# Optimization experiments

Hardware: AMD Instinct MI355X
Metric: run time of the kernel (lower is better)

## Reference

```python
import jax, jax.numpy as jnp
import numpy as np

N = 100000
E = 3200000
IN_DIM = 128
HID = 64
BN_EPS = 1e-5


def _gcn_conv(x, W, b, src, dst, dinv):
    h = x @ W                                      # [N, out]
    coeff = (dinv[src] * dinv[dst])[:, None]       # [E, 1]
    msg = h[src] * coeff                           # gather over edges
    agg = jax.ops.segment_sum(msg, dst, num_segments=N)
    agg = agg + h * (dinv * dinv)[:, None]         # self-loop term
    return agg + b


def setup_inputs() -> dict:
    key = jax.random.key(0)
    ks = jax.random.split(key, 12)
    x = jax.random.normal(ks[0], (N, IN_DIM), dtype=jnp.float32)
    edge_index = jax.random.randint(ks[1], (2, E), 0, N, dtype=jnp.int64)
    s1 = 1.0 / np.sqrt(IN_DIM)
    s2 = 1.0 / np.sqrt(HID)
    W1 = jax.random.uniform(ks[2], (IN_DIM, HID), jnp.float32, -s1, s1)
    b1 = jnp.zeros((HID,), jnp.float32)
    W2 = jax.random.uniform(ks[3], (HID, HID), jnp.float32, -s2, s2)
    b2 = jnp.zeros((HID,), jnp.float32)
    W3 = jax.random.uniform(ks[4], (HID, 1), jnp.float32, -s2, s2)
    b3 = jnp.zeros((1,), jnp.float32)
    g1 = jnp.ones((HID,), jnp.float32)
    beta1 = jnp.zeros((HID,), jnp.float32)
    m1 = 0.1 * jax.random.normal(ks[5], (HID,), jnp.float32)
    v1 = jax.random.uniform(ks[6], (HID,), jnp.float32) + 0.5
    g2 = jnp.ones((HID,), jnp.float32)
    beta2 = jnp.zeros((HID,), jnp.float32)
    m2 = 0.1 * jax.random.normal(ks[7], (HID,), jnp.float32)
    v2 = jax.random.uniform(ks[8], (HID,), jnp.float32) + 0.5
    return {"x": x, "edge_index": edge_index,
            "W1": W1, "b1": b1, "W2": W2, "b2": b2, "W3": W3, "b3": b3,
            "g1": g1, "beta1": beta1, "m1": m1, "v1": v1,
            "g2": g2, "beta2": beta2, "m2": m2, "v2": v2}


def reference(x, edge_index, W1, b1, W2, b2, W3, b3,
              g1, beta1, m1, v1, g2, beta2, m2, v2):
    src, dst = edge_index[0], edge_index[1]
    # degree with self-loops (computed on destination index, PyG convention)
    deg = jax.ops.segment_sum(jnp.ones((E,), jnp.float32), dst, num_segments=N) + 1.0
    dinv = jax.lax.rsqrt(deg)

    def bn(h, g, beta, m, v):
        return (h - m) * jax.lax.rsqrt(v + BN_EPS) * g + beta

    h = _gcn_conv(x, W1, b1, src, dst, dinv)
    h = jax.nn.relu(bn(h, g1, beta1, m1, v1))  # dropout is a no-op in eval
    h = _gcn_conv(h, W2, b2, src, dst, dinv)
    h = jax.nn.relu(bn(h, g2, beta2, m2, v2))
    h = _gcn_conv(h, W3, b3, src, dst, dinv)
    return jax.nn.sigmoid(h)  # [N, 1]
```

## Files before the change

kernel.cpp:

```cpp
#include <hip/hip_runtime.h>
#include <math.h>

#define N_NODES 100000
#define E_EDGES 3200000
#define IN_DIM_ 128
#define HID_ 64
#define BN_EPS_ 1e-5f

#define PB 200
#define CHUNK 16000
#define NBUCK 391

typedef __attribute__((ext_vector_type(8))) short short8;
typedef __attribute__((ext_vector_type(4))) float f32x4;

__device__ inline ushort f2bf(float f) {
    union { float f; unsigned u; } c; c.f = f;
    unsigned r = c.u + 0x7fff + ((c.u >> 16) & 1);
    return (ushort)(r >> 16);
}
__device__ inline float bf_lo(unsigned p) { union { unsigned u; float f; } c; c.u = p << 16; return c.f; }
__device__ inline float bf_hi(unsigned p) { union { unsigned u; float f; } c; c.u = p & 0xffff0000u; return c.f; }

__global__ __launch_bounds__(256) void passA1_hist(const int* __restrict__ ei,
                                                   int* __restrict__ histPB) {
    __shared__ int hist[NBUCK];
    int t = threadIdx.x, b = blockIdx.x;
    for (int k = t; k < NBUCK; k += 256) hist[k] = 0;
    __syncthreads();
    int e0 = b * CHUNK, e1 = e0 + CHUNK;
    for (int e = e0 + t; e < e1; e += 256) {
        int d = ei[E_EDGES + e];
        atomicAdd(&hist[d >> 8], 1);
    }
    __syncthreads();
    for (int k = t; k < NBUCK; k += 256) histPB[k * PB + b] = hist[k];
}

__global__ __launch_bounds__(256) void scan_rows(int* __restrict__ histPB,
                                                 int* __restrict__ bucket_tot) {
    __shared__ int wsum[4];
    int k = blockIdx.x, t = threadIdx.x, lane = t & 63, wv = t >> 6;
    int v = (t < PB) ? histPB[k * PB + t] : 0;
    int s = v;
#pragma unroll
    for (int off = 1; off < 64; off <<= 1) {
        int u = __shfl_up(s, off, 64);
        if (lane >= off) s += u;
    }
    if (lane == 63) wsum[wv] = s;
    __syncthreads();
    int wbase = 0;
    for (int w = 0; w < wv; w++) wbase += wsum[w];
    if (t < PB) histPB[k * PB + t] = wbase + s - v;
    if (t == 255) bucket_tot[k] = wbase + s;
}

__global__ __launch_bounds__(512) void scan_totals(const int* __restrict__ bucket_tot,
                                                   int* __restrict__ bucket_base,
                                                   int* __restrict__ row_ptr) {
    __shared__ int wsum[8];
    int t = threadIdx.x, lane = t & 63, wv = t >> 6;
    int v = (t < NBUCK) ? bucket_tot[t] : 0;
    int s = v;
#pragma unroll
    for (int off = 1; off < 64; off <<= 1) {
        int u = __shfl_up(s, off, 64);
        if (lane >= off) s += u;
    }
    if (lane == 63) wsum[wv] = s;
    __syncthreads();
    int wbase = 0;
    for (int w = 0; w < wv; w++) wbase += wsum[w];
    if (t < NBUCK) bucket_base[t] = wbase + s - v;
    if (t == 0) {
        bucket_base[NBUCK] = E_EDGES;
        row_ptr[N_NODES] = E_EDGES;
    }
}

__global__ __launch_bounds__(256) void passA2_scatter(const int* __restrict__ ei,
                                                      const int* __restrict__ histPB,
                                                      const int* __restrict__ bucket_base,
                                                      int* __restrict__ ebuf) {
    __shared__ int cur[NBUCK];
    int t = threadIdx.x, b = blockIdx.x;
    for (int k = t; k < NBUCK; k += 256) cur[k] = bucket_base[k] + histPB[k * PB + b];
    __syncthreads();
    int e0 = b * CHUNK, e1 = e0 + CHUNK;
    for (int e = e0 + t; e < e1; e += 256) {
        int s = ei[e];
        int d = ei[E_EDGES + e];
        int bk = d >> 8;
        int pos = atomicAdd(&cur[bk], 1);
        ebuf[pos] = s | ((d & 255) << 17);
    }
}

__global__ __launch_bounds__(256) void passB_place(const int* __restrict__ ebuf,
                                                   const int* __restrict__ bucket_base,
                                                   int* __restrict__ row_ptr,
                                                   int* __restrict__ csr_src,
                                                   float* __restrict__ dinv) {
    __shared__ int hist[256];
    __shared__ int wsum[4];
    int b = blockIdx.x, t = threadIdx.x, lane = t & 63, wv = t >> 6;
    int base = bucket_base[b], end = bucket_base[b + 1];
    hist[t] = 0;
    __syncthreads();
    for (int k = base + t; k < end; k += 256)
        atomicAdd(&hist[ebuf[k] >> 17], 1);
    __syncthreads();
    int v = hist[t];
    int s = v;
#pragma unroll
    for (int off = 1; off < 64; off <<= 1) {
        int u = __shfl_up(s, off, 64);
        if (lane >= off) s += u;
    }
    if (lane == 63) wsum[wv] = s;
    __syncthreads();
    int wbase = 0;
    for (int w = 0; w < wv; w++) wbase += wsum[w];
    int excl = wbase + s - v;
    int node = b * 256 + t;
    if (node < N_NODES) {
        row_ptr[node] = base + excl;
        dinv[node] = rsqrtf((float)v + 1.0f);
    }
    __syncthreads();
    hist[t] = excl;
    __syncthreads();
    for (int k = base + t; k < end; k += 256) {
        int pv = ebuf[k];
        int pos = atomicAdd(&hist[pv >> 17], 1);
        csr_src[base + pos] = pv & 0x1FFFF;
    }
}

template<int K, bool BF16IN>
__global__ __launch_bounds__(256) void gemm_bf16(const void* __restrict__ Xv,
                                                 const float* __restrict__ W,
                                                 const float* __restrict__ dinv,
                                                 ushort* __restrict__ hs) {
    constexpr int KP = K + 8;
    __shared__ ushort A_lds[64][KP];
    __shared__ ushort Wt_lds[64][KP];
    int t = threadIdx.x;
    long row0 = (long)blockIdx.x * 64;

    for (int i = t; i < K * 16; i += 256) {
        float4 w4 = ((const float4*)W)[i];
        int k = i >> 4, n = (i & 15) * 4;
        Wt_lds[n + 0][k] = f2bf(w4.x);
        Wt_lds[n + 1][k] = f2bf(w4.y);
        Wt_lds[n + 2][k] = f2bf(w4.z);
        Wt_lds[n + 3][k] = f2bf(w4.w);
    }
    if (BF16IN) {
        constexpr int K2 = K / 2;
        const unsigned* X = (const unsigned*)Xv;
        for (int i = t; i < 64 * K2; i += 256) {
            int r = i / K2, c = i % K2;
            unsigned val = 0;
            long row = row0 + r;
            if (row < N_NODES) val = X[row * K2 + c];
            *(unsigned*)&A_lds[r][c * 2] = val;
        }
    } else {
        constexpr int K4 = K / 4;
        const float* X = (const float*)Xv;
        for (int i = t; i < 64 * K4; i += 256) {
            int r = i / K4, c = i % K4;
            float4 val = make_float4(0.f, 0.f, 0.f, 0.f);
            long row = row0 + r;
            if (row < N_NODES) val = ((const float4*)X)[row * K4 + c];
            int cb = c * 4;
            A_lds[r][cb + 0] = f2bf(val.x);
            A_lds[r][cb + 1] = f2bf(val.y);
            A_lds[r][cb + 2] = f2bf(val.z);
            A_lds[r][cb + 3] = f2bf(val.w);
        }
    }
    __syncthreads();

    int w = t >> 6, l = t & 63;
    int m = l & 15, quad = l >> 4;
    f32x4 acc[4];
#pragma unroll
    for (int c = 0; c < 4; c++) acc[c] = (f32x4){0.f, 0.f, 0.f, 0.f};

#pragma unroll
    for (int ch = 0; ch < K / 32; ch++) {
        short8 a = *(const short8*)&A_lds[16 * w + m][32 * ch + 8 * quad];
#pragma unroll
        for (int c = 0; c < 4; c++) {
            short8 b = *(const short8*)&Wt_lds[16 * c + m][32 * ch + 8 * quad];
            acc[c] = __builtin_amdgcn_mfma_f32_16x16x32_bf16(a, b, acc[c], 0, 0, 0);
        }
    }

#pragma unroll
    for (int r = 0; r < 4; r++) {
        long node = row0 + 16 * w + quad * 4 + r;
        if (node < N_NODES) {
            float dv = dinv[node];
#pragma unroll
            for (int c = 0; c < 4; c++)
                hs[node * 64 + 16 * c + m] = f2bf(acc[c][r] * dv);
        }
    }
}

template<bool LAST>
__global__ __launch_bounds__(256) void gather_feat(const int* __restrict__ row_ptr,
                                                   const int* __restrict__ csr_src,
                                                   const ushort* __restrict__ hs,
                                                   const float* __restrict__ dinv,
                                                   const float* __restrict__ b,
                                                   const float* __restrict__ g,
                                                   const float* __restrict__ beta,
                                                   const float* __restrict__ m,
                                                   const float* __restrict__ v,
                                                   unsigned* __restrict__ y,
                                                   const float* __restrict__ W3,
                                                   float* __restrict__ hs3, int n) {
    int i = (blockIdx.x * 256 + threadIdx.x) >> 6;
    if (i >= n) return;
    int l = threadIdx.x & 63;
    int half = l >> 5, u = l & 31;
    const unsigned* H = (const unsigned*)hs;
    int beg = row_ptr[i], end = row_ptr[i + 1];
    float a0 = 0.f, a1 = 0.f;
    int k = beg + half;
    for (; k + 6 < end; k += 8) {
        int s0 = csr_src[k], s1 = csr_src[k + 2], s2 = csr_src[k + 4], s3 = csr_src[k + 6];
        unsigned p0 = H[s0 * 32 + u], p1 = H[s1 * 32 + u];
        unsigned p2 = H[s2 * 32 + u], p3 = H[s3 * 32 + u];
        a0 += (bf_lo(p0) + bf_lo(p1)) + (bf_lo(p2) + bf_lo(p3));
        a1 += (bf_hi(p0) + bf_hi(p1)) + (bf_hi(p2) + bf_hi(p3));
    }
    for (; k < end; k += 2) {
        unsigned p = H[csr_src[k] * 32 + u];
        a0 += bf_lo(p);
        a1 += bf_hi(p);
    }
    a0 += __shfl_xor(a0, 32, 64);
    a1 += __shfl_xor(a1, 32, 64);
    unsigned ps = H[(long)i * 32 + u];
    a0 += bf_lo(ps);
    a1 += bf_hi(ps);

    float2 bb = ((const float2*)b)[u];
    float2 gg = ((const float2*)g)[u];
    float2 be = ((const float2*)beta)[u];
    float2 mm = ((const float2*)m)[u];
    float2 vv = ((const float2*)v)[u];
    float di = dinv[i];
    float s0 = gg.x * rsqrtf(vv.x + BN_EPS_);
    float s1 = gg.y * rsqrtf(vv.y + BN_EPS_);
    float o0 = fmaxf((di * a0 + bb.x - mm.x) * s0 + be.x, 0.f);
    float o1 = fmaxf((di * a1 + bb.y - mm.y) * s1 + be.y, 0.f);

    if (LAST) {
        float2 w3 = ((const float2*)W3)[u];
        float p = o0 * w3.x + o1 * w3.y;
#pragma unroll
        for (int off = 16; off > 0; off >>= 1)
            p += __shfl_down(p, off, 32);
        if (l == 0) hs3[i] = p * di;
    } else {
        if (half == 0)
            y[(long)i * 32 + u] = (unsigned)f2bf(o0) | ((unsigned)f2bf(o1) << 16);
    }
}

__global__ __launch_bounds__(256) void gather3(const int* __restrict__ row_ptr,
                                               const int* __restrict__ csr_src,
                                               const float* __restrict__ hs3,
                                               const float* __restrict__ dinv,
                                               const float* __restrict__ b3,
                                               float* __restrict__ out, int n) {
    int i = blockIdx.x * 256 + threadIdx.x;
    if (i >= n) return;
    int beg = row_ptr[i], end = row_ptr[i + 1];
    float s0 = hs3[i], s1 = 0.f, s2 = 0.f, s3 = 0.f;
    float s4 = 0.f, s5 = 0.f, s6 = 0.f, s7 = 0.f;
    int k = beg;
    for (; k + 8 <= end; k += 8) {
        s0 += hs3[csr_src[k]];
        s1 += hs3[csr_src[k + 1]];
        s2 += hs3[csr_src[k + 2]];
        s3 += hs3[csr_src[k + 3]];
        s4 += hs3[csr_src[k + 4]];
        s5 += hs3[csr_src[k + 5]];
        s6 += hs3[csr_src[k + 6]];
        s7 += hs3[csr_src[k + 7]];
    }
    for (; k < end; k++) s0 += hs3[csr_src[k]];
    float z = dinv[i] * (((s0 + s1) + (s2 + s3)) + ((s4 + s5) + (s6 + s7))) + b3[0];
    out[i] = 1.f / (1.f + expf(-z));
}

extern "C" void kernel_launch(void* const* d_in, const int* in_sizes, int n_in,
                              void* d_out, int out_size, void* d_ws, size_t ws_size,
                              hipStream_t stream) {
    const int N = N_NODES;
    const int E = E_EDGES;

    const float* x   = (const float*)d_in[0];
    const int*   ei  = (const int*)d_in[1];
    const float* W1  = (const float*)d_in[2];
    const float* b1  = (const float*)d_in[3];
    const float* W2  = (const float*)d_in[4];
    const float* b2  = (const float*)d_in[5];
    const float* W3  = (const float*)d_in[6];
    const float* b3  = (const float*)d_in[7];
    const float* g1  = (const float*)d_in[8];
    const float* bt1 = (const float*)d_in[9];
    const float* m1  = (const float*)d_in[10];
    const float* v1  = (const float*)d_in[11];
    const float* g2  = (const float*)d_in[12];
    const float* bt2 = (const float*)d_in[13];
    const float* m2  = (const float*)d_in[14];
    const float* v2  = (const float*)d_in[15];
    float* out = (float*)d_out;

    int*    wsi         = (int*)d_ws;
    float*  dinv        = (float*)wsi;
    float*  hs3         = (float*)(wsi + (long)N);
    int*    row_ptr     = wsi + 2L * N;
    int*    histPB      = wsi + 3L * N + 16;
    int*    bucket_tot  = histPB + NBUCK * PB;
    int*    bucket_base = bucket_tot + 400;
    int*    csr_src     = bucket_base + 400;
    ushort* hsb         = (ushort*)(csr_src + (long)E);
    unsigned* yb        = (unsigned*)(csr_src + (long)E + 32L * N);
    int*    ebuf        = (int*)hsb;

    passA1_hist<<<PB, 256, 0, stream>>>(ei, histPB);
    scan_rows<<<NBUCK, 256, 0, stream>>>(histPB, bucket_tot);
    scan_totals<<<1, 512, 0, stream>>>(bucket_tot, bucket_base, row_ptr);
    passA2_scatter<<<PB, 256, 0, stream>>>(ei, histPB, bucket_base, ebuf);
    passB_place<<<NBUCK, 256, 0, stream>>>(ebuf, bucket_base, row_ptr, csr_src, dinv);

    gemm_bf16<IN_DIM_, false><<<(N + 63) / 64, 256, 0, stream>>>(x, W1, dinv, hsb);
    gather_feat<false><<<N / 4, 256, 0, stream>>>(row_ptr, csr_src, hsb, dinv,
                                                  b1, g1, bt1, m1, v1, yb, W3, hs3, N);
    gemm_bf16<HID_, true><<<(N + 63) / 64, 256, 0, stream>>>(yb, W2, dinv, hsb);
    gather_feat<true><<<N / 4, 256, 0, stream>>>(row_ptr, csr_src, hsb, dinv,
                                                 b2, g2, bt2, m2, v2, yb, W3, hs3, N);
    gather3<<<(N + 255) / 256, 256, 0, stream>>>(row_ptr, csr_src, hs3, dinv, b3, out, N);
}
```

Before: 435.1 us.

## Sort CSR neighbors by source range and unroll gather loop to 8 loads

The CSR placement pass now sub-buckets each destination node's edges into six source-index ranges, so neighbor lists come out roughly ordered by source node. Gathers across the wave then hit nearby rows of the feature table at about the same time, which should improve L2 locality. The aggregation loop is also unrolled from 4 to 8 outstanding gathers per half-wave to raise memory-level parallelism. Costs are a larger LDS histogram, an integer divide per edge in the placement pass, and more registers in the aggregation kernel.

```diff
diff --git a/kernel.cpp b/kernel.cpp
--- a/kernel.cpp
+++ b/kernel.cpp
@@ -10,6 +10,9 @@
 #define PB 200
 #define CHUNK 16000
 #define NBUCK 391
+
+#define CCH 6
+#define CNODES 16667
 
 typedef __attribute__((ext_vector_type(8))) short short8;
 typedef __attribute__((ext_vector_type(4))) float f32x4;
@@ -102,17 +105,24 @@
                                                    int* __restrict__ row_ptr,
                                                    int* __restrict__ csr_src,
                                                    float* __restrict__ dinv) {
-    __shared__ int hist[256];
+    __shared__ int hist[256 * CCH];
     __shared__ int wsum[4];
     int b = blockIdx.x, t = threadIdx.x, lane = t & 63, wv = t >> 6;
     int base = bucket_base[b], end = bucket_base[b + 1];
-    hist[t] = 0;
-    __syncthreads();
-    for (int k = base + t; k < end; k += 256)
-        atomicAdd(&hist[ebuf[k] >> 17], 1);
-    __syncthreads();
-    int v = hist[t];
-    int s = v;
+    for (int k = t; k < 256 * CCH; k += 256) hist[k] = 0;
+    __syncthreads();
+    for (int k = base + t; k < end; k += 256) {
+        int pv = ebuf[k];
+        int nd = (pv >> 17) & 255;
+        int c = (pv & 0x1FFFF) / CNODES;
+        atomicAdd(&hist[nd * CCH + c], 1);
+    }
+    __syncthreads();
+    int v[CCH];
+    int tot = 0;
+#pragma unroll
+    for (int c = 0; c < CCH; c++) { v[c] = hist[t * CCH + c]; tot += v[c]; }
+    int s = tot;
 #pragma unroll
     for (int off = 1; off < 64; off <<= 1) {
         int u = __shfl_up(s, off, 64);
@@ -122,18 +132,24 @@
     __syncthreads();
     int wbase = 0;
     for (int w = 0; w < wv; w++) wbase += wsum[w];
-    int excl = wbase + s - v;
+    int excl = wbase + s - tot;
     int node = b * 256 + t;
     if (node < N_NODES) {
         row_ptr[node] = base + excl;
-        dinv[node] = rsqrtf((float)v + 1.0f);
-    }
-    __syncthreads();
-    hist[t] = excl;
+        dinv[node] = rsqrtf((float)tot + 1.0f);
+    }
+    int run = excl;
+#pragma unroll
+    for (int c = 0; c < CCH; c++) {
+        hist[t * CCH + c] = run;
+        run += v[c];
+    }
     __syncthreads();
     for (int k = base + t; k < end; k += 256) {
         int pv = ebuf[k];
-        int pos = atomicAdd(&hist[pv >> 17], 1);
+        int nd = (pv >> 17) & 255;
+        int c = (pv & 0x1FFFF) / CNODES;
+        int pos = atomicAdd(&hist[nd * CCH + c], 1);
         csr_src[base + pos] = pv & 0x1FFFF;
     }
 }
@@ -233,12 +249,17 @@
     int beg = row_ptr[i], end = row_ptr[i + 1];
     float a0 = 0.f, a1 = 0.f;
     int k = beg + half;
-    for (; k + 6 < end; k += 8) {
-        int s0 = csr_src[k], s1 = csr_src[k + 2], s2 = csr_src[k + 4], s3 = csr_src[k + 6];
+    for (; k + 14 < end; k += 16) {
+        int s0 = csr_src[k],      s1 = csr_src[k + 2],  s2 = csr_src[k + 4],  s3 = csr_src[k + 6];
+        int s4 = csr_src[k + 8],  s5 = csr_src[k + 10], s6 = csr_src[k + 12], s7 = csr_src[k + 14];
         unsigned p0 = H[s0 * 32 + u], p1 = H[s1 * 32 + u];
         unsigned p2 = H[s2 * 32 + u], p3 = H[s3 * 32 + u];
-        a0 += (bf_lo(p0) + bf_lo(p1)) + (bf_lo(p2) + bf_lo(p3));
-        a1 += (bf_hi(p0) + bf_hi(p1)) + (bf_hi(p2) + bf_hi(p3));
+        unsigned p4 = H[s4 * 32 + u], p5 = H[s5 * 32 + u];
+        unsigned p6 = H[s6 * 32 + u], p7 = H[s7 * 32 + u];
+        a0 += ((bf_lo(p0) + bf_lo(p1)) + (bf_lo(p2) + bf_lo(p3))) +
+              ((bf_lo(p4) + bf_lo(p5)) + (bf_lo(p6) + bf_lo(p7)));
+        a1 += ((bf_hi(p0) + bf_hi(p1)) + (bf_hi(p2) + bf_hi(p3))) +
+              ((bf_hi(p4) + bf_hi(p5)) + (bf_hi(p6) + bf_hi(p7)));
     }
     for (; k < end; k += 2) {
         unsigned p = H[csr_src[k] * 32 + u];
```

Measured after the change: 438.6 us. Within noise of the previous version (+0.8%).

## Gather 16-byte feature slices over 8 edges per wave in GCN aggregation

Applied to the files above, without the earlier changes.

Restructures the per-node gather so each 64-lane wave processes 8 edges at once, with each lane loading a 16-byte uint4 slice (8 bf16 features) rather than 4 bytes. Partial sums are combined across edge slots with xor shuffles, and the bias, batch-norm and output stages are widened to match. The aim is fewer, wider memory requests and more edges in flight per iteration for low-degree nodes. The cost is more registers and a longer shuffle reduction, and lanes sit idle in the tail when a node's degree is not a multiple of 8.

```diff
diff --git a/kernel.cpp b/kernel.cpp
--- a/kernel.cpp
+++ b/kernel.cpp
@@ -228,50 +228,94 @@
     int i = (blockIdx.x * 256 + threadIdx.x) >> 6;
     if (i >= n) return;
     int l = threadIdx.x & 63;
-    int half = l >> 5, u = l & 31;
-    const unsigned* H = (const unsigned*)hs;
+    int es = l >> 3, fg = l & 7;
+    const uint4* H4 = (const uint4*)hs;
+
+    float a0 = 0.f, a1 = 0.f, a2 = 0.f, a3 = 0.f;
+    float a4 = 0.f, a5 = 0.f, a6 = 0.f, a7 = 0.f;
+
+    if (es == 0) {
+        uint4 p = H4[(long)i * 8 + fg];
+        a0 += bf_lo(p.x); a1 += bf_hi(p.x);
+        a2 += bf_lo(p.y); a3 += bf_hi(p.y);
+        a4 += bf_lo(p.z); a5 += bf_hi(p.z);
+        a6 += bf_lo(p.w); a7 += bf_hi(p.w);
+    }
+
     int beg = row_ptr[i], end = row_ptr[i + 1];
-    float a0 = 0.f, a1 = 0.f;
-    int k = beg + half;
-    for (; k + 6 < end; k += 8) {
-        int s0 = csr_src[k], s1 = csr_src[k + 2], s2 = csr_src[k + 4], s3 = csr_src[k + 6];
-        unsigned p0 = H[s0 * 32 + u], p1 = H[s1 * 32 + u];
-        unsigned p2 = H[s2 * 32 + u], p3 = H[s3 * 32 + u];
-        a0 += (bf_lo(p0) + bf_lo(p1)) + (bf_lo(p2) + bf_lo(p3));
-        a1 += (bf_hi(p0) + bf_hi(p1)) + (bf_hi(p2) + bf_hi(p3));
-    }
-    for (; k < end; k += 2) {
-        unsigned p = H[csr_src[k] * 32 + u];
-        a0 += bf_lo(p);
-        a1 += bf_hi(p);
-    }
-    a0 += __shfl_xor(a0, 32, 64);
-    a1 += __shfl_xor(a1, 32, 64);
-    unsigned ps = H[(long)i * 32 + u];
-    a0 += bf_lo(ps);
-    a1 += bf_hi(ps);
-
-    float2 bb = ((const float2*)b)[u];
-    float2 gg = ((const float2*)g)[u];
-    float2 be = ((const float2*)beta)[u];
-    float2 mm = ((const float2*)m)[u];
-    float2 vv = ((const float2*)v)[u];
+    int k = beg;
+    for (; k + 16 <= end; k += 16) {
+        int sA = csr_src[k + es];
+        int sB = csr_src[k + 8 + es];
+        uint4 pA = H4[(long)sA * 8 + fg];
+        uint4 pB = H4[(long)sB * 8 + fg];
+        a0 += bf_lo(pA.x) + bf_lo(pB.x); a1 += bf_hi(pA.x) + bf_hi(pB.x);
+        a2 += bf_lo(pA.y) + bf_lo(pB.y); a3 += bf_hi(pA.y) + bf_hi(pB.y);
+        a4 += bf_lo(pA.z) + bf_lo(pB.z); a5 += bf_hi(pA.z) + bf_hi(pB.z);
+        a6 += bf_lo(pA.w) + bf_lo(pB.w); a7 += bf_hi(pA.w) + bf_hi(pB.w);
+    }
+    for (; k + 8 <= end; k += 8) {
+        int s = csr_src[k + es];
+        uint4 p = H4[(long)s * 8 + fg];
+        a0 += bf_lo(p.x); a1 += bf_hi(p.x);
+        a2 += bf_lo(p.y); a3 += bf_hi(p.y);
+        a4 += bf_lo(p.z); a5 += bf_hi(p.z);
+        a6 += bf_lo(p.w); a7 += bf_hi(p.w);
+    }
+    int rem = end - k;
+    if (es < rem) {
+        int s = csr_src[k + es];
+        uint4 p = H4[(long)s * 8 + fg];
+        a0 += bf_lo(p.x); a1 += bf_hi(p.x);
+        a2 += bf_lo(p.y); a3 += bf_hi(p.y);
+        a4 += bf_lo(p.z); a5 += bf_hi(p.z);
+        a6 += bf_lo(p.w); a7 += bf_hi(p.w);
+    }
+
+#pragma unroll
+    for (int off = 8; off < 64; off <<= 1) {
+        a0 += __shfl_xor(a0, off, 64);
+        a1 += __shfl_xor(a1, off, 64);
+        a2 += __shfl_xor(a2, off, 64);
+        a3 += __shfl_xor(a3, off, 64);
+        a4 += __shfl_xor(a4, off, 64);
+        a5 += __shfl_xor(a5, off, 64);
+        a6 += __shfl_xor(a6, off, 64);
+        a7 += __shfl_xor(a7, off, 64);
+    }
+
+    float4 bb0 = ((const float4*)b)[fg * 2],    bb1 = ((const float4*)b)[fg * 2 + 1];
+    float4 gg0 = ((const float4*)g)[fg * 2],    gg1 = ((const float4*)g)[fg * 2 + 1];
+    float4 be0 = ((const float4*)beta)[fg * 2], be1 = ((const float4*)beta)[fg * 2 + 1];
+    float4 mm0 = ((const float4*)m)[fg * 2],    mm1 = ((const float4*)m)[fg * 2 + 1];
+    float4 vv0 = ((const float4*)v)[fg * 2],    vv1 = ((const float4*)v)[fg * 2 + 1];
     float di = dinv[i];
-    float s0 = gg.x * rsqrtf(vv.x + BN_EPS_);
-    float s1 = gg.y * rsqrtf(vv.y + BN_EPS_);
-    float o0 = fmaxf((di * a0 + bb.x - mm.x) * s0 + be.x, 0.f);
-    float o1 = fmaxf((di * a1 + bb.y - mm.y) * s1 + be.y, 0.f);
+    float o0 = fmaxf((di * a0 + bb0.x - mm0.x) * (gg0.x * rsqrtf(vv0.x + BN_EPS_)) + be0.x, 0.f);
+    float o1 = fmaxf((di * a1 + bb0.y - mm0.y) * (gg0.y * rsqrtf(vv0.y + BN_EPS_)) + be0.y, 0.f);
+    float o2 = fmaxf((di * a2 + bb0.z - mm0.z) * (gg0.z * rsqrtf(vv0.z + BN_EPS_)) + be0.z, 0.f);
+    float o3 = fmaxf((di * a3 + bb0.w - mm0.w) * (gg0.w * rsqrtf(vv0.w + BN_EPS_)) + be0.w, 0.f);
+    float o4 = fmaxf((di * a4 + bb1.x - mm1.x) * (gg1.x * rsqrtf(vv1.x + BN_EPS_)) + be1.x, 0.f);
+    float o5 = fmaxf((di * a5 + bb1.y - mm1.y) * (gg1.y * rsqrtf(vv1.y + BN_EPS_)) + be1.y, 0.f);
+    float o6 = fmaxf((di * a6 + bb1.z - mm1.z) * (gg1.z * rsqrtf(vv1.z + BN_EPS_)) + be1.z, 0.f);
+    float o7 = fmaxf((di * a7 + bb1.w - mm1.w) * (gg1.w * rsqrtf(vv1.w + BN_EPS_)) + be1.w, 0.f);
 
     if (LAST) {
-        float2 w3 = ((const float2*)W3)[u];
-        float p = o0 * w3.x + o1 * w3.y;
-#pragma unroll
-        for (int off = 16; off > 0; off >>= 1)
-            p += __shfl_down(p, off, 32);
+        float4 w30 = ((const float4*)W3)[fg * 2], w31 = ((const float4*)W3)[fg * 2 + 1];
+        float p = o0 * w30.x + o1 * w30.y + o2 * w30.z + o3 * w30.w +
+                  o4 * w31.x + o5 * w31.y + o6 * w31.z + o7 * w31.w;
+#pragma unroll
+        for (int off = 1; off < 8; off <<= 1)
+            p += __shfl_xor(p, off, 64);
         if (l == 0) hs3[i] = p * di;
     } else {
-        if (half == 0)
-            y[(long)i * 32 + u] = (unsigned)f2bf(o0) | ((unsigned)f2bf(o1) << 16);
+        if (es == 0) {
+            uint4 pk;
+            pk.x = (unsigned)f2bf(o0) | ((unsigned)f2bf(o1) << 16);
+            pk.y = (unsigned)f2bf(o2) | ((unsigned)f2bf(o3) << 16);
+            pk.z = (unsigned)f2bf(o4) | ((unsigned)f2bf(o5) << 16);
+            pk.w = (unsigned)f2bf(o6) | ((unsigned)f2bf(o7) << 16);
+            ((uint4*)y)[(long)i * 8 + fg] = pk;
+        }
     }
 }
 
```

Result: no change. 432.1 us (-0.7%).
